# Optimization experiments

Measured on AMD Instinct MI355X. Metric: run time of the kernel, lower is better.

Reference implementation:

```python
import jax, jax.numpy as jnp
import numpy as np

D_MODEL = 192   # embed_dim
DEPTH = 24
D_INNER = 384   # expand=2 * d_model
D_STATE = 16
D_CONV = 4
DT_RANK = 12    # ceil(192/16)
B = 8
IMG = 224
P = 16          # patch size / stride


def setup_inputs() -> dict:
    key = jax.random.key(0)
    ks = jax.random.split(key, 10)
    s = lambda k, shp, sc=0.02: jax.random.normal(k, shp, jnp.float32) * sc
    return {
        "x": jax.random.normal(ks[0], (B, 3, IMG, IMG), jnp.float32),
        "pe_w": s(ks[1], (D_MODEL, 3, P, P)),
        "pe_b": jnp.zeros((D_MODEL,), jnp.float32),
        "norm_w": jnp.ones((DEPTH, D_MODEL), jnp.float32),
        "norm_b": jnp.zeros((DEPTH, D_MODEL), jnp.float32),
        "in_proj_w": s(ks[2], (DEPTH, 2 * D_INNER, D_MODEL)),
        "conv_w": s(ks[3], (DEPTH, D_INNER, D_CONV), 0.1),
        "conv_b": jnp.zeros((DEPTH, D_INNER), jnp.float32),
        "xproj_w": s(ks[4], (DEPTH, DT_RANK + 2 * D_STATE, D_INNER)),
        "dtproj_w": s(ks[5], (DEPTH, D_INNER, DT_RANK), 0.1),
        "dtproj_b": s(ks[6], (DEPTH, D_INNER), 0.1),
        "A_log": jnp.broadcast_to(jnp.log(jnp.arange(1.0, D_STATE + 1.0, dtype=jnp.float32)), (DEPTH, D_INNER, D_STATE)).astype(jnp.float32),
        "D_param": jnp.ones((DEPTH, D_INNER), jnp.float32),
        "outproj_w": s(ks[7], (DEPTH, D_MODEL, D_INNER)),
        "normf_w": jnp.ones((D_MODEL,), jnp.float32),
        "normf_b": jnp.zeros((D_MODEL,), jnp.float32),
    }


def _layernorm(x, w, b, eps=1e-5):
    mu = x.mean(-1, keepdims=True)
    var = ((x - mu) ** 2).mean(-1, keepdims=True)
    return (x - mu) * jax.lax.rsqrt(var + eps) * w + b


def _causal_dwconv(x, w, b):
    # x: [B, L, d_inner]; depthwise causal conv1d (mamba conv1d, padding=d_conv-1, truncated to L)
    xt = jnp.pad(x.swapaxes(1, 2), ((0, 0), (0, 0), (D_CONV - 1, 0)))  # [B, di, L+3]
    y = jax.lax.conv_general_dilated(xt, w[:, None, :], (1,), 'VALID',
                                     feature_group_count=w.shape[0])
    return (y + b[:, None]).swapaxes(1, 2)  # [B, L, di]


def _selective_scan(u, dt, Bm, Cm, A, Dp):
    # u, dt: [B, L, di]; Bm, Cm: [B, L, ds]; A: [di, ds]; Dp: [di]
    dA = jnp.exp(dt[..., None] * A)                         # [B, L, di, ds]
    dBu = (dt * u)[..., None] * Bm[:, :, None, :]           # [B, L, di, ds]

    def step(h, inp):
        dA_t, dBu_t, C_t = inp
        h = dA_t * h + dBu_t                                # [B, di, ds]
        return h, jnp.einsum('bds,bs->bd', h, C_t)

    h0 = jnp.zeros((u.shape[0], A.shape[0], A.shape[1]), u.dtype)
    _, ys = jax.lax.scan(step, h0,
                         (dA.swapaxes(0, 1), dBu.swapaxes(0, 1), Cm.swapaxes(0, 1)))
    return ys.swapaxes(0, 1) + u * Dp                       # [B, L, di]


def _mamba(x, ipw, cw, cb, xpw, dtw, dtb, Alog, Dp, opw):
    xz = jnp.einsum('bld,ed->ble', x, ipw)                  # [B, L, 2*di]
    xin, z = jnp.split(xz, 2, axis=-1)
    xin = jax.nn.silu(_causal_dwconv(xin, cw, cb))
    xdbl = jnp.einsum('bld,ed->ble', xin, xpw)              # [B, L, dt_rank+2*ds]
    dt = jax.nn.softplus(jnp.einsum('blr,dr->bld', xdbl[..., :DT_RANK], dtw) + dtb)
    Bm = xdbl[..., DT_RANK:DT_RANK + D_STATE]
    Cm = xdbl[..., DT_RANK + D_STATE:]
    A = -jnp.exp(Alog)
    y = _selective_scan(xin, dt, Bm, Cm, A, Dp)
    y = y * jax.nn.silu(z)
    return jnp.einsum('bld,ed->ble', y, opw)                # [B, L, D]


def reference(x, pe_w, pe_b, norm_w, norm_b, in_proj_w, conv_w, conv_b,
              xproj_w, dtproj_w, dtproj_b, A_log, D_param, outproj_w,
              normf_w, normf_b):
    # PatchEmbed: conv stride 16 -> flatten -> [B, 196, 192]
    feat = jax.lax.conv_general_dilated(x, pe_w, (P, P), 'VALID') + pe_b[None, :, None, None]
    h = feat.reshape(feat.shape[0], D_MODEL, -1).swapaxes(1, 2)
    residual = None
    for i in range(DEPTH):
        residual = h if residual is None else residual + h
        hn = _layernorm(residual, norm_w[i], norm_b[i])
        h = _mamba(hn, in_proj_w[i], conv_w[i], conv_b[i], xproj_w[i],
                   dtproj_w[i], dtproj_b[i], A_log[i], D_param[i], outproj_w[i])
    residual = residual + h
    return _layernorm(residual, normf_w, normf_b)           # [B, 196, 192]
```

## Files before the change

### kernel.cpp

```cpp
#include <hip/hip_runtime.h>
#include <hip/hip_bf16.h>


#define NTOK   1568
#define DMODEL 192
#define DINNER 384
#define DSTATE 16
#define DTRANK 12
#define DEPTH  24
#define LSEQ   196
#define TCH    49

typedef __attribute__((ext_vector_type(8))) short short8;
typedef __attribute__((ext_vector_type(4))) float floatx4;

__device__ inline short f2bf(float f) {
    __hip_bfloat16 h = __float2bfloat16(f);
    return *reinterpret_cast<short*>(&h);
}

__global__ __launch_bounds__(256) void im2col(
    const float* __restrict__ x, __hip_bfloat16* __restrict__ patches)
{
    int idx = blockIdx.x * 256 + threadIdx.x;
    if (idx >= NTOK * 768) return;
    int tok = idx / 768, e = idx % 768;
    int b = tok / LSEQ, l = tok % LSEQ;
    int py = l / 14, px = l % 14;
    int ic = e >> 8, rem = e & 255, ky = rem >> 4, kx = rem & 15;
    patches[idx] = __float2bfloat16(x[((b * 3 + ic) * 224 + py * 16 + ky) * 224 + px * 16 + kx]);
}

#define LDA 40

__global__ __launch_bounds__(256) void gemm_in(
    const __hip_bfloat16* __restrict__ A, const float* __restrict__ W,
    float* __restrict__ C, int M, int N, int K)
{
    __shared__ short As[64 * LDA];
    __shared__ short Ws[64 * LDA];
    int tid = threadIdx.x;
    int m0 = blockIdx.x * 64, n0 = blockIdx.y * 64;
    int wv = tid >> 6, lane = tid & 63;
    int fm = lane & 15, q = lane >> 4;
    int row = tid >> 2, kc = (tid & 3) * 8;
    floatx4 acc[4];
#pragma unroll
    for (int nt = 0; nt < 4; ++nt) acc[nt] = (floatx4){0.f, 0.f, 0.f, 0.f};

    for (int k0 = 0; k0 < K; k0 += 32) {
        {
            int m = m0 + row;
            short8 v = {0,0,0,0,0,0,0,0};
            if (m < M) v = *(const short8*)&A[(size_t)m * K + k0 + kc];
            *(short8*)&As[row * LDA + kc] = v;
        }
        {
            int n = n0 + row;
            float4 b0 = *(const float4*)&W[(size_t)n * K + k0 + kc];
            float4 b1 = *(const float4*)&W[(size_t)n * K + k0 + kc + 4];
            short8 v;
            v[0]=f2bf(b0.x); v[1]=f2bf(b0.y); v[2]=f2bf(b0.z); v[3]=f2bf(b0.w);
            v[4]=f2bf(b1.x); v[5]=f2bf(b1.y); v[6]=f2bf(b1.z); v[7]=f2bf(b1.w);
            *(short8*)&Ws[row * LDA + kc] = v;
        }
        __syncthreads();
        short8 af = *(const short8*)&As[(wv * 16 + fm) * LDA + q * 8];
#pragma unroll
        for (int nt = 0; nt < 4; ++nt) {
            short8 bf = *(const short8*)&Ws[(nt * 16 + fm) * LDA + q * 8];
            acc[nt] = __builtin_amdgcn_mfma_f32_16x16x32_bf16(af, bf, acc[nt], 0, 0, 0);
        }
        __syncthreads();
    }
#pragma unroll
    for (int nt = 0; nt < 4; ++nt) {
        int col = n0 + nt * 16 + fm;
#pragma unroll
        for (int r = 0; r < 4; ++r) {
            int mrow = m0 + wv * 16 + q * 4 + r;
            if (mrow < M) C[(size_t)mrow * N + col] = acc[nt][r];
        }
    }
}

__global__ __launch_bounds__(256) void gemm_ln(
    const __hip_bfloat16* __restrict__ A, const float* __restrict__ W,
    const float* __restrict__ bias, float* __restrict__ residual,
    __hip_bfloat16* __restrict__ hn, float* __restrict__ outf,
    const float* __restrict__ lnw, const float* __restrict__ lnb,
    int K, int accumulate)
{
    __shared__ short As[16 * LDA];
    __shared__ short Ws[192 * LDA];
    __shared__ float slw[192], slb[192], sbias[192];
    __shared__ float sS1[4][16], sS2[4][16];
    int tid = threadIdx.x;
    int m0 = blockIdx.x * 16;
    int wv = tid >> 6, lane = tid & 63;
    int fm = lane & 15, q = lane >> 4;
    int wrow = tid >> 2, kc = (tid & 3) * 8;
    if (tid < 192) {
        slw[tid] = lnw[tid];
        slb[tid] = lnb[tid];
        sbias[tid] = bias ? bias[tid] : 0.f;
    }
    floatx4 acc[3];
#pragma unroll
    for (int j = 0; j < 3; ++j) acc[j] = (floatx4){0.f, 0.f, 0.f, 0.f};

    short8 aR = {0,0,0,0,0,0,0,0};
    float4 b0[3], b1[3];
    if (tid < 64) aR = *(const short8*)&A[(size_t)(m0 + (tid >> 2)) * K + kc];
#pragma unroll
    for (int j = 0; j < 3; ++j) {
        int n = wrow + 64 * j;
        b0[j] = *(const float4*)&W[(size_t)n * K + kc];
        b1[j] = *(const float4*)&W[(size_t)n * K + kc + 4];
    }

    for (int k0 = 0; k0 < K; k0 += 32) {
        if (tid < 64) *(short8*)&As[(tid >> 2) * LDA + kc] = aR;
#pragma unroll
        for (int j = 0; j < 3; ++j) {
            int n = wrow + 64 * j;
            short8 v;
            v[0]=f2bf(b0[j].x); v[1]=f2bf(b0[j].y); v[2]=f2bf(b0[j].z); v[3]=f2bf(b0[j].w);
            v[4]=f2bf(b1[j].x); v[5]=f2bf(b1[j].y); v[6]=f2bf(b1[j].z); v[7]=f2bf(b1[j].w);
            *(short8*)&Ws[n * LDA + kc] = v;
        }
        __syncthreads();
        int kn = k0 + 32;
        if (kn < K) {
            if (tid < 64) aR = *(const short8*)&A[(size_t)(m0 + (tid >> 2)) * K + kn + kc];
#pragma unroll
            for (int j = 0; j < 3; ++j) {
                int n = wrow + 64 * j;
                b0[j] = *(const float4*)&W[(size_t)n * K + kn + kc];
                b1[j] = *(const float4*)&W[(size_t)n * K + kn + kc + 4];
            }
        }
        short8 af = *(const short8*)&As[fm * LDA + q * 8];
#pragma unroll
        for (int j = 0; j < 3; ++j) {
            int ct = wv * 3 + j;
            short8 bf = *(const short8*)&Ws[(ct * 16 + fm) * LDA + q * 8];
            acc[j] = __builtin_amdgcn_mfma_f32_16x16x32_bf16(af, bf, acc[j], 0, 0, 0);
        }
        __syncthreads();
    }

    float v[3][4];
#pragma unroll
    for (int r = 0; r < 4; ++r) {
        int m = m0 + q * 4 + r;
#pragma unroll
        for (int j = 0; j < 3; ++j) {
            int col = (wv * 3 + j) * 16 + fm;
            float t = acc[j][r] + sbias[col];
            if (accumulate) t += residual[(size_t)m * DMODEL + col];
            v[j][r] = t;
        }
    }
#pragma unroll
    for (int r = 0; r < 4; ++r) {
        int m = m0 + q * 4 + r;
#pragma unroll
        for (int j = 0; j < 3; ++j)
            residual[(size_t)m * DMODEL + (wv * 3 + j) * 16 + fm] = v[j][r];
    }
#pragma unroll
    for (int r = 0; r < 4; ++r) {
        float s1 = v[0][r] + v[1][r] + v[2][r];
        float s2 = v[0][r]*v[0][r] + v[1][r]*v[1][r] + v[2][r]*v[2][r];
        s1 += __shfl_xor(s1, 1); s2 += __shfl_xor(s2, 1);
        s1 += __shfl_xor(s1, 2); s2 += __shfl_xor(s2, 2);
        s1 += __shfl_xor(s1, 4); s2 += __shfl_xor(s2, 4);
        s1 += __shfl_xor(s1, 8); s2 += __shfl_xor(s2, 8);
        if (fm == 0) { sS1[wv][q * 4 + r] = s1; sS2[wv][q * 4 + r] = s2; }
    }
    __syncthreads();
#pragma unroll
    for (int r = 0; r < 4; ++r) {
        int row = q * 4 + r;
        int m = m0 + row;
        float S1 = sS1[0][row] + sS1[1][row] + sS1[2][row] + sS1[3][row];
        float S2 = sS2[0][row] + sS2[1][row] + sS2[2][row] + sS2[3][row];
        float mean = S1 * (1.f / DMODEL);
        float var  = S2 * (1.f / DMODEL) - mean * mean;
        float rstd = rsqrtf(var + 1e-5f);
#pragma unroll
        for (int j = 0; j < 3; ++j) {
            int col = (wv * 3 + j) * 16 + fm;
            float o = (v[j][r] - mean) * rstd * slw[col] + slb[col];
            if (outf) outf[(size_t)m * DMODEL + col] = o;
            else      hn[(size_t)m * DMODEL + col] = __float2bfloat16(o);
        }
    }
}

__global__ __launch_bounds__(256) void conv_xproj_dt(
    const float* __restrict__ xz, const float* __restrict__ cw,
    const float* __restrict__ cb, const float* __restrict__ xpw,
    const float* __restrict__ dtw, const float* __restrict__ dtb,
    float* __restrict__ u, float* __restrict__ dtg, float* __restrict__ bcg)
{
    __shared__ float su[DINNER];
    __shared__ float sx[44];
    int blk = blockIdx.x;
    int b = blk / LSEQ, l = blk % LSEQ;
    int tid = threadIdx.x;
    for (int d = tid; d < DINNER; d += 256) {
        float acc = cb[d];
#pragma unroll
        for (int k = 0; k < 4; ++k) {
            int li = l - 3 + k;
            if (li >= 0) acc += xz[(size_t)(b * LSEQ + li) * 768 + d] * cw[d * 4 + k];
        }
        float sig = 1.f / (1.f + __expf(-acc));
        float val = acc * sig;
        su[d] = val;
        u[(size_t)(b * LSEQ + l) * DINNER + d] = val;
    }
    __syncthreads();
    if (tid < 176) {
        int e = tid >> 2, p = tid & 3;
        float acc = 0.f;
        const float* wr = &xpw[e * DINNER + p * 96];
        const float* ur = &su[p * 96];
#pragma unroll 8
        for (int j = 0; j < 96; ++j) acc += ur[j] * wr[j];
        acc += __shfl_xor(acc, 1);
        acc += __shfl_xor(acc, 2);
        if (p == 0) sx[e] = acc;
    }
    __syncthreads();
    for (int d = tid; d < DINNER; d += 256) {
        float acc = dtb[d];
#pragma unroll
        for (int r = 0; r < DTRANK; ++r) acc += sx[r] * dtw[d * DTRANK + r];
        float sp = (acc > 20.f) ? acc : log1pf(__expf(acc));
        dtg[(size_t)(b * LSEQ + l) * DINNER + d] = sp;
    }
    if (tid < 32) bcg[(b * LSEQ + l) * 32 + tid] = sx[DTRANK + tid];
}

#define SPAD 272
__global__ __launch_bounds__(256) void scan_kernel(
    const float* __restrict__ u, const float* __restrict__ dtg,
    const float* __restrict__ bc, const float* __restrict__ xz,
    const float* __restrict__ Alog, const float* __restrict__ Dp,
    __hip_bfloat16* __restrict__ y)
{
    __shared__ float sdt[TCH][16];
    __shared__ float su_[TCH][16];
    __shared__ float sz_[TCH][16];
    __shared__ float sB_[TCH][16];
    __shared__ float sC_[TCH][16];
    __shared__ float sprod[TCH][SPAD];

    int b  = blockIdx.x / 24;
    int dg = blockIdx.x % 24;
    int tid = threadIdx.x;
    int s = tid & 15, dl = tid >> 4;
    int d = dg * 16 + dl;
    float Ads = -expf(Alog[d * DSTATE + s]);
    float Dd2 = Dp[dg * 16 + (tid & 15)];
    float h = 0.f;

    for (int c0 = 0; c0 < LSEQ; c0 += TCH) {
        if (tid < TCH * 4) {
            int t = tid >> 2, j4 = (tid & 3) * 4;
            size_t tok = (size_t)(b * LSEQ + c0 + t);
            *(float4*)&sdt[t][j4] = *(const float4*)&dtg[tok * DINNER + dg * 16 + j4];
            *(float4*)&su_[t][j4] = *(const float4*)&u  [tok * DINNER + dg * 16 + j4];
            *(float4*)&sz_[t][j4] = *(const float4*)&xz [tok * 768 + DINNER + dg * 16 + j4];
            *(float4*)&sB_[t][j4] = *(const float4*)&bc [tok * 32 + j4];
            *(float4*)&sC_[t][j4] = *(const float4*)&bc [tok * 32 + 16 + j4];
        }
        __syncthreads();

#pragma unroll 7
        for (int t = 0; t < TCH; ++t) {
            float dtv = sdt[t][dl];
            float uv  = su_[t][dl];
            float Bv  = sB_[t][s];
            float Cv  = sC_[t][s];
            float dA  = __expf(dtv * Ads);
            h = dA * h + (dtv * uv) * Bv;
            sprod[t][dl * 17 + s] = h * Cv;
        }
        __syncthreads();

        for (int i = tid; i < TCH * 16; i += 256) {
            int t = i >> 4, dl2 = i & 15;
            float sum = 0.f;
#pragma unroll
            for (int j = 0; j < 16; ++j) sum += sprod[t][dl2 * 17 + j];
            float uv = su_[t][dl2];
            float zv = sz_[t][dl2];
            float sig = 1.f / (1.f + __expf(-zv));
            y[(size_t)(b * LSEQ + c0 + t) * DINNER + dg * 16 + dl2] =
                __float2bfloat16((sum + uv * Dd2) * (zv * sig));
        }
        __syncthreads();
    }
}

extern "C" void kernel_launch(void* const* d_in, const int* in_sizes, int n_in,
                              void* d_out, int out_size, void* d_ws, size_t ws_size,
                              hipStream_t stream)
{
    const float* x         = (const float*)d_in[0];
    const float* pe_w      = (const float*)d_in[1];
    const float* pe_b      = (const float*)d_in[2];
    const float* norm_w    = (const float*)d_in[3];
    const float* norm_b    = (const float*)d_in[4];
    const float* in_proj_w = (const float*)d_in[5];
    const float* conv_w    = (const float*)d_in[6];
    const float* conv_b    = (const float*)d_in[7];
    const float* xproj_w   = (const float*)d_in[8];
    const float* dtproj_w  = (const float*)d_in[9];
    const float* dtproj_b  = (const float*)d_in[10];
    const float* A_log     = (const float*)d_in[11];
    const float* D_param   = (const float*)d_in[12];
    const float* outproj_w = (const float*)d_in[13];
    const float* normf_w   = (const float*)d_in[14];
    const float* normf_b   = (const float*)d_in[15];

    float* ws = (float*)d_ws;
    float* residual = ws;
    float* xz       = residual + 301056;
    float* ubuf     = xz + 1204224;
    float* dtbuf    = ubuf + 602112;
    float* bcbuf    = dtbuf + 602112;
    __hip_bfloat16* hn  = (__hip_bfloat16*)(bcbuf + 50176);
    __hip_bfloat16* ybf = hn + 301056;
    __hip_bfloat16* patches = (__hip_bfloat16*)ubuf;

    im2col<<<(NTOK * 768 + 255) / 256, 256, 0, stream>>>(x, patches);
    gemm_ln<<<98, 256, 0, stream>>>(
        patches, pe_w, pe_b, residual, hn, nullptr,
        norm_w, norm_b, 768, 0);

    for (int i = 0; i < DEPTH; ++i) {
        int last = (i == DEPTH - 1);
        gemm_in<<<dim3(25, 12), 256, 0, stream>>>(
            hn, in_proj_w + (size_t)i * 768 * DMODEL, xz, NTOK, 768, DMODEL);
        conv_xproj_dt<<<NTOK, 256, 0, stream>>>(
            xz, conv_w + (size_t)i * DINNER * 4, conv_b + (size_t)i * DINNER,
            xproj_w + (size_t)i * 44 * DINNER, dtproj_w + (size_t)i * DINNER * DTRANK,
            dtproj_b + (size_t)i * DINNER, ubuf, dtbuf, bcbuf);
        scan_kernel<<<192, 256, 0, stream>>>(
            ubuf, dtbuf, bcbuf, xz, A_log + (size_t)i * DINNER * DSTATE,
            D_param + (size_t)i * DINNER, ybf);
        gemm_ln<<<98, 256, 0, stream>>>(
            ybf, outproj_w + (size_t)i * DMODEL * DINNER, nullptr, residual, hn,
            last ? (float*)d_out : nullptr,
            last ? normf_w : norm_w + (i + 1) * DMODEL,
            last ? normf_b : norm_b + (i + 1) * DMODEL,
            DINNER, 1);
    }
}
```

Before: 1.551 ms.

## Pre-convert weights to bf16, drop LDS staging in GEMMs, batch x_proj with MFMA

Adds a one-time kernel per call that converts in_proj, out_proj, patch-embed and (zero-padded) x_proj weights to bf16. The GEMMs then read bf16 operands straight from global memory into MFMA fragments, with no LDS staging or barriers, and use templated K so the loops fully unroll. conv_xproj_dt now handles 14 tokens per block and computes the x_proj with bf16 MFMA instead of per-token scalar dot products. The aim is to cut per-layer fp32→bf16 conversion, LDS traffic and launch granularity. In exchange it adds a conversion pass every call, lowers x_proj precision to bf16, and relies on cache-served uncoalesced global fragment loads.

```diff
diff --git a/kernel.cpp b/kernel.cpp
--- a/kernel.cpp
+++ b/kernel.cpp
@@ -12,11 +12,46 @@
 #define TCH    49
 
 typedef __attribute__((ext_vector_type(8))) short short8;
+typedef __attribute__((ext_vector_type(4))) short short4v;
 typedef __attribute__((ext_vector_type(4))) float floatx4;
 
 __device__ inline short f2bf(float f) {
     __hip_bfloat16 h = __float2bfloat16(f);
     return *reinterpret_cast<short*>(&h);
+}
+
+#define CVT_N1 884736
+#define CVT_N2 442368
+#define CVT_N3 36864
+#define CVT_N4 110592
+__global__ __launch_bounds__(256) void cvt_weights(
+    const float* __restrict__ inw, const float* __restrict__ outw,
+    const float* __restrict__ pew, const float* __restrict__ xpw,
+    short* __restrict__ w_in, short* __restrict__ w_out,
+    short* __restrict__ w_pe, short* __restrict__ w_xp)
+{
+    int idx = blockIdx.x * 256 + threadIdx.x;
+    float4 v;
+    short* dst;
+    if (idx < CVT_N1) {
+        v = ((const float4*)inw)[idx]; dst = w_in + (size_t)idx * 4;
+    } else if (idx < CVT_N1 + CVT_N2) {
+        int i = idx - CVT_N1;
+        v = ((const float4*)outw)[i]; dst = w_out + (size_t)i * 4;
+    } else if (idx < CVT_N1 + CVT_N2 + CVT_N3) {
+        int i = idx - CVT_N1 - CVT_N2;
+        v = ((const float4*)pew)[i]; dst = w_pe + (size_t)i * 4;
+    } else {
+        int i = idx - CVT_N1 - CVT_N2 - CVT_N3;
+        int layer = i / 4608, rr = i % 4608;
+        int row = rr / 96, c4 = (rr % 96) * 4;
+        if (row < 44) v = *(const float4*)&xpw[((size_t)layer * 44 + row) * 384 + c4];
+        else          v = make_float4(0.f, 0.f, 0.f, 0.f);
+        dst = w_xp + ((size_t)layer * 48 + row) * 384 + c4;
+    }
+    short4v o;
+    o[0] = f2bf(v.x); o[1] = f2bf(v.y); o[2] = f2bf(v.z); o[3] = f2bf(v.w);
+    *(short4v*)dst = o;
 }
 
 __global__ __launch_bounds__(256) void im2col(
@@ -31,47 +66,29 @@
     patches[idx] = __float2bfloat16(x[((b * 3 + ic) * 224 + py * 16 + ky) * 224 + px * 16 + kx]);
 }
 
-#define LDA 40
-
+template<int K>
 __global__ __launch_bounds__(256) void gemm_in(
-    const __hip_bfloat16* __restrict__ A, const float* __restrict__ W,
-    float* __restrict__ C, int M, int N, int K)
-{
-    __shared__ short As[64 * LDA];
-    __shared__ short Ws[64 * LDA];
+    const __hip_bfloat16* __restrict__ A, const short* __restrict__ Wb,
+    float* __restrict__ C, int M, int N)
+{
     int tid = threadIdx.x;
     int m0 = blockIdx.x * 64, n0 = blockIdx.y * 64;
     int wv = tid >> 6, lane = tid & 63;
     int fm = lane & 15, q = lane >> 4;
-    int row = tid >> 2, kc = (tid & 3) * 8;
+    int m = m0 + wv * 16 + fm;
+    const short* Ab = (const short*)A;
     floatx4 acc[4];
 #pragma unroll
     for (int nt = 0; nt < 4; ++nt) acc[nt] = (floatx4){0.f, 0.f, 0.f, 0.f};
-
+#pragma unroll
     for (int k0 = 0; k0 < K; k0 += 32) {
-        {
-            int m = m0 + row;
-            short8 v = {0,0,0,0,0,0,0,0};
-            if (m < M) v = *(const short8*)&A[(size_t)m * K + k0 + kc];
-            *(short8*)&As[row * LDA + kc] = v;
-        }
-        {
-            int n = n0 + row;
-            float4 b0 = *(const float4*)&W[(size_t)n * K + k0 + kc];
-            float4 b1 = *(const float4*)&W[(size_t)n * K + k0 + kc + 4];
-            short8 v;
-            v[0]=f2bf(b0.x); v[1]=f2bf(b0.y); v[2]=f2bf(b0.z); v[3]=f2bf(b0.w);
-            v[4]=f2bf(b1.x); v[5]=f2bf(b1.y); v[6]=f2bf(b1.z); v[7]=f2bf(b1.w);
-            *(short8*)&Ws[row * LDA + kc] = v;
-        }
-        __syncthreads();
-        short8 af = *(const short8*)&As[(wv * 16 + fm) * LDA + q * 8];
+        short8 af = {0,0,0,0,0,0,0,0};
+        if (m < M) af = *(const short8*)&Ab[(size_t)m * K + k0 + q * 8];
 #pragma unroll
         for (int nt = 0; nt < 4; ++nt) {
-            short8 bf = *(const short8*)&Ws[(nt * 16 + fm) * LDA + q * 8];
+            short8 bf = *(const short8*)&Wb[(size_t)(n0 + nt * 16 + fm) * K + k0 + q * 8];
             acc[nt] = __builtin_amdgcn_mfma_f32_16x16x32_bf16(af, bf, acc[nt], 0, 0, 0);
         }
-        __syncthreads();
     }
 #pragma unroll
     for (int nt = 0; nt < 4; ++nt) {
@@ -84,71 +101,40 @@
     }
 }
 
+template<int K>
 __global__ __launch_bounds__(256) void gemm_ln(
-    const __hip_bfloat16* __restrict__ A, const float* __restrict__ W,
+    const __hip_bfloat16* __restrict__ A, const short* __restrict__ Wb,
     const float* __restrict__ bias, float* __restrict__ residual,
     __hip_bfloat16* __restrict__ hn, float* __restrict__ outf,
     const float* __restrict__ lnw, const float* __restrict__ lnb,
-    int K, int accumulate)
-{
-    __shared__ short As[16 * LDA];
-    __shared__ short Ws[192 * LDA];
+    int accumulate)
+{
     __shared__ float slw[192], slb[192], sbias[192];
     __shared__ float sS1[4][16], sS2[4][16];
     int tid = threadIdx.x;
     int m0 = blockIdx.x * 16;
     int wv = tid >> 6, lane = tid & 63;
     int fm = lane & 15, q = lane >> 4;
-    int wrow = tid >> 2, kc = (tid & 3) * 8;
     if (tid < 192) {
         slw[tid] = lnw[tid];
         slb[tid] = lnb[tid];
         sbias[tid] = bias ? bias[tid] : 0.f;
     }
+    const short* Ab = (const short*)A;
     floatx4 acc[3];
 #pragma unroll
     for (int j = 0; j < 3; ++j) acc[j] = (floatx4){0.f, 0.f, 0.f, 0.f};
-
-    short8 aR = {0,0,0,0,0,0,0,0};
-    float4 b0[3], b1[3];
-    if (tid < 64) aR = *(const short8*)&A[(size_t)(m0 + (tid >> 2)) * K + kc];
-#pragma unroll
-    for (int j = 0; j < 3; ++j) {
-        int n = wrow + 64 * j;
-        b0[j] = *(const float4*)&W[(size_t)n * K + kc];
-        b1[j] = *(const float4*)&W[(size_t)n * K + kc + 4];
-    }
-
+#pragma unroll
     for (int k0 = 0; k0 < K; k0 += 32) {
-        if (tid < 64) *(short8*)&As[(tid >> 2) * LDA + kc] = aR;
+        short8 af = *(const short8*)&Ab[(size_t)(m0 + fm) * K + k0 + q * 8];
 #pragma unroll
         for (int j = 0; j < 3; ++j) {
-            int n = wrow + 64 * j;
-            short8 v;
-            v[0]=f2bf(b0[j].x); v[1]=f2bf(b0[j].y); v[2]=f2bf(b0[j].z); v[3]=f2bf(b0[j].w);
-            v[4]=f2bf(b1[j].x); v[5]=f2bf(b1[j].y); v[6]=f2bf(b1[j].z); v[7]=f2bf(b1[j].w);
-            *(short8*)&Ws[n * LDA + kc] = v;
-        }
-        __syncthreads();
-        int kn = k0 + 32;
-        if (kn < K) {
-            if (tid < 64) aR = *(const short8*)&A[(size_t)(m0 + (tid >> 2)) * K + kn + kc];
-#pragma unroll
-            for (int j = 0; j < 3; ++j) {
-                int n = wrow + 64 * j;
-                b0[j] = *(const float4*)&W[(size_t)n * K + kn + kc];
-                b1[j] = *(const float4*)&W[(size_t)n * K + kn + kc + 4];
-            }
-        }
-        short8 af = *(const short8*)&As[fm * LDA + q * 8];
-#pragma unroll
-        for (int j = 0; j < 3; ++j) {
-            int ct = wv * 3 + j;
-            short8 bf = *(const short8*)&Ws[(ct * 16 + fm) * LDA + q * 8];
+            int n = (wv * 3 + j) * 16 + fm;
+            short8 bf = *(const short8*)&Wb[(size_t)n * K + k0 + q * 8];
             acc[j] = __builtin_amdgcn_mfma_f32_16x16x32_bf16(af, bf, acc[j], 0, 0, 0);
         }
-        __syncthreads();
-    }
+    }
+    __syncthreads();
 
     float v[3][4];
 #pragma unroll
@@ -201,48 +187,77 @@
 
 __global__ __launch_bounds__(256) void conv_xproj_dt(
     const float* __restrict__ xz, const float* __restrict__ cw,
-    const float* __restrict__ cb, const float* __restrict__ xpw,
+    const float* __restrict__ cb, const short* __restrict__ xpb,
     const float* __restrict__ dtw, const float* __restrict__ dtb,
     float* __restrict__ u, float* __restrict__ dtg, float* __restrict__ bcg)
 {
-    __shared__ float su[DINNER];
-    __shared__ float sx[44];
-    int blk = blockIdx.x;
-    int b = blk / LSEQ, l = blk % LSEQ;
+    __shared__ short su16[16 * 392];
+    __shared__ float sx[14 * 48];
+    int bx = blockIdx.x;
+    int b = bx / 14, c = bx % 14;
+    int l0 = c * 14;
     int tid = threadIdx.x;
-    for (int d = tid; d < DINNER; d += 256) {
+
+    for (int idx = tid; idx < 14 * 384; idx += 256) {
+        int t = idx / 384, d = idx % 384;
+        int l = l0 + t;
+        size_t tok = (size_t)(b * LSEQ + l);
+        float4 w4 = *(const float4*)&cw[d * 4];
         float acc = cb[d];
-#pragma unroll
-        for (int k = 0; k < 4; ++k) {
-            int li = l - 3 + k;
-            if (li >= 0) acc += xz[(size_t)(b * LSEQ + li) * 768 + d] * cw[d * 4 + k];
-        }
+        int li = l - 3;
+        if (li >= 0)     acc += xz[(size_t)(b * LSEQ + li    ) * 768 + d] * w4.x;
+        if (li + 1 >= 0) acc += xz[(size_t)(b * LSEQ + li + 1) * 768 + d] * w4.y;
+        if (li + 2 >= 0) acc += xz[(size_t)(b * LSEQ + li + 2) * 768 + d] * w4.z;
+        acc += xz[tok * 768 + d] * w4.w;
         float sig = 1.f / (1.f + __expf(-acc));
         float val = acc * sig;
-        su[d] = val;
-        u[(size_t)(b * LSEQ + l) * DINNER + d] = val;
+        u[tok * 384 + d] = val;
+        su16[t * 392 + d] = f2bf(val);
+    }
+    for (int idx = tid; idx < 2 * 384; idx += 256) {
+        int t = 14 + idx / 384, d = idx % 384;
+        su16[t * 392 + d] = 0;
     }
     __syncthreads();
-    if (tid < 176) {
-        int e = tid >> 2, p = tid & 3;
-        float acc = 0.f;
-        const float* wr = &xpw[e * DINNER + p * 96];
-        const float* ur = &su[p * 96];
-#pragma unroll 8
-        for (int j = 0; j < 96; ++j) acc += ur[j] * wr[j];
-        acc += __shfl_xor(acc, 1);
-        acc += __shfl_xor(acc, 2);
-        if (p == 0) sx[e] = acc;
+
+    int wv = tid >> 6, lane = tid & 63;
+    int fm = lane & 15, q = lane >> 4;
+    if (wv < 3) {
+        floatx4 acc = {0.f, 0.f, 0.f, 0.f};
+#pragma unroll
+        for (int ks = 0; ks < 12; ++ks) {
+            short8 af = *(const short8*)&su16[fm * 392 + ks * 32 + q * 8];
+            short8 bf = *(const short8*)&xpb[(size_t)(wv * 16 + fm) * 384 + ks * 32 + q * 8];
+            acc = __builtin_amdgcn_mfma_f32_16x16x32_bf16(af, bf, acc, 0, 0, 0);
+        }
+#pragma unroll
+        for (int r = 0; r < 4; ++r) {
+            int t = q * 4 + r;
+            if (t < 14) sx[t * 48 + wv * 16 + fm] = acc[r];
+        }
     }
     __syncthreads();
-    for (int d = tid; d < DINNER; d += 256) {
-        float acc = dtb[d];
-#pragma unroll
-        for (int r = 0; r < DTRANK; ++r) acc += sx[r] * dtw[d * DTRANK + r];
-        float sp = (acc > 20.f) ? acc : log1pf(__expf(acc));
-        dtg[(size_t)(b * LSEQ + l) * DINNER + d] = sp;
-    }
-    if (tid < 32) bcg[(b * LSEQ + l) * 32 + tid] = sx[DTRANK + tid];
+
+    for (int d = tid; d < 384; d += 256) {
+        float4 wa = *(const float4*)&dtw[d * 12];
+        float4 wb = *(const float4*)&dtw[d * 12 + 4];
+        float4 wc = *(const float4*)&dtw[d * 12 + 8];
+        float bias = dtb[d];
+#pragma unroll
+        for (int t = 0; t < 14; ++t) {
+            const float* sxr = &sx[t * 48];
+            float a = bias;
+            a += sxr[0]*wa.x + sxr[1]*wa.y + sxr[2] *wa.z + sxr[3] *wa.w;
+            a += sxr[4]*wb.x + sxr[5]*wb.y + sxr[6] *wb.z + sxr[7] *wb.w;
+            a += sxr[8]*wc.x + sxr[9]*wc.y + sxr[10]*wc.z + sxr[11]*wc.w;
+            float sp = (a > 20.f) ? a : log1pf(__expf(a));
+            dtg[(size_t)(b * LSEQ + l0 + t) * 384 + d] = sp;
+        }
+    }
+    if (tid < 448) {
+        int t = tid >> 5, j = tid & 31;
+        bcg[(size_t)(b * LSEQ + l0 + t) * 32 + j] = sx[t * 48 + 12 + j];
+    }
 }
 
 #define SPAD 272
@@ -334,31 +349,37 @@
     float* ubuf     = xz + 1204224;
     float* dtbuf    = ubuf + 602112;
     float* bcbuf    = dtbuf + 602112;
-    __hip_bfloat16* hn  = (__hip_bfloat16*)(bcbuf + 50176);
-    __hip_bfloat16* ybf = hn + 301056;
-    __hip_bfloat16* patches = (__hip_bfloat16*)ubuf;
+    __hip_bfloat16* hn      = (__hip_bfloat16*)(ws + 2759680);
+    __hip_bfloat16* ybf     = (__hip_bfloat16*)(ws + 2910208);
+    __hip_bfloat16* patches = (__hip_bfloat16*)(ws + 3211264);
+    short* w_in  = (short*)(ws + 3813376);
+    short* w_out = (short*)(ws + 5582848);
+    short* w_pe  = (short*)(ws + 6467584);
+    short* w_xp  = (short*)(ws + 6541312);
+
+    cvt_weights<<<5760, 256, 0, stream>>>(
+        in_proj_w, outproj_w, pe_w, xproj_w, w_in, w_out, w_pe, w_xp);
 
     im2col<<<(NTOK * 768 + 255) / 256, 256, 0, stream>>>(x, patches);
-    gemm_ln<<<98, 256, 0, stream>>>(
-        patches, pe_w, pe_b, residual, hn, nullptr,
-        norm_w, norm_b, 768, 0);
+    gemm_ln<768><<<98, 256, 0, stream>>>(
+        patches, w_pe, pe_b, residual, hn, nullptr, norm_w, norm_b, 0);
 
     for (int i = 0; i < DEPTH; ++i) {
         int last = (i == DEPTH - 1);
-        gemm_in<<<dim3(25, 12), 256, 0, stream>>>(
-            hn, in_proj_w + (size_t)i * 768 * DMODEL, xz, NTOK, 768, DMODEL);
-        conv_xproj_dt<<<NTOK, 256, 0, stream>>>(
+        gemm_in<192><<<dim3(25, 12), 256, 0, stream>>>(
+            hn, w_in + (size_t)i * 768 * DMODEL, xz, NTOK, 768);
+        conv_xproj_dt<<<112, 256, 0, stream>>>(
             xz, conv_w + (size_t)i * DINNER * 4, conv_b + (size_t)i * DINNER,
-            xproj_w + (size_t)i * 44 * DINNER, dtproj_w + (size_t)i * DINNER * DTRANK,
+            w_xp + (size_t)i * 48 * DINNER, dtproj_w + (size_t)i * DINNER * DTRANK,
             dtproj_b + (size_t)i * DINNER, ubuf, dtbuf, bcbuf);
         scan_kernel<<<192, 256, 0, stream>>>(
             ubuf, dtbuf, bcbuf, xz, A_log + (size_t)i * DINNER * DSTATE,
             D_param + (size_t)i * DINNER, ybf);
-        gemm_ln<<<98, 256, 0, stream>>>(
-            ybf, outproj_w + (size_t)i * DMODEL * DINNER, nullptr, residual, hn,
+        gemm_ln<384><<<98, 256, 0, stream>>>(
+            ybf, w_out + (size_t)i * DMODEL * DINNER, nullptr, residual, hn,
             last ? (float*)d_out : nullptr,
             last ? normf_w : norm_w + (i + 1) * DMODEL,
             last ? normf_b : norm_b + (i + 1) * DMODEL,
-            DINNER, 1);
-    }
-}
+            1);
+    }
+}
```

Result: slower. 1.835 ms (+18.3%).
